# Kernel optimization log

Measured on AMD Instinct MI355X. Metric: run time of the kernel, lower is better.

## Reference

```python
import jax, jax.numpy as jnp
import numpy as np

H, W = 200, 200           # BEV spatial shape (single level)
NBQ, NH, NL, NP = 2, 8, 1, 4
D = 256
HD = D // NH


def setup_inputs() -> dict:
    key = jax.random.key(0)
    ks = jax.random.split(key, 12)
    bs, nq = 1, H * W
    query = jax.random.normal(ks[0], (bs, nq, D), jnp.float32)
    value = jax.random.normal(ks[1], (bs, NBQ * nq, D), jnp.float32)
    reference_points = jax.random.uniform(ks[2], (bs, nq, NL, 2), dtype=jnp.float32)
    spatial_shapes = jnp.array([[H, W]], dtype=jnp.int32)
    sc = 1.0 / np.sqrt(D)
    W_v = jax.random.normal(ks[3], (D, D), jnp.float32) * sc
    b_v = jax.random.normal(ks[4], (D,), jnp.float32) * 0.01
    W_so = jax.random.normal(ks[5], (2 * D, NBQ * NH * NL * NP * 2), jnp.float32) * 0.02
    b_so = jax.random.normal(ks[6], (NBQ * NH * NL * NP * 2,), jnp.float32) * 0.5
    W_aw = jax.random.normal(ks[7], (2 * D, NBQ * NH * NL * NP), jnp.float32) * 0.02
    b_aw = jax.random.normal(ks[8], (NBQ * NH * NL * NP,), jnp.float32) * 0.01
    W_o = jax.random.normal(ks[9], (D, D), jnp.float32) * sc
    b_o = jax.random.normal(ks[10], (D,), jnp.float32) * 0.01
    return {"query": query, "value": value, "reference_points": reference_points,
            "spatial_shapes": spatial_shapes,
            "W_v": W_v, "b_v": b_v, "W_so": W_so, "b_so": b_so,
            "W_aw": W_aw, "b_aw": b_aw, "W_o": W_o, "b_o": b_o}


def _ms_deform_attn(value, locs, attn):
    # value: (B, K, NH, HD); locs: (B, nq, NH, NL, NP, 2) in [0,1]; attn: (B, nq, NH, NL, NP)
    B, K, h, d = value.shape
    nq = locs.shape[1]
    out = jnp.zeros((B, nq, h, d), value.dtype)
    start = 0
    for l, (Hl, Wl) in enumerate([(H, W)]):
        v = value[:, start:start + Hl * Wl].transpose(0, 2, 1, 3).reshape(B * h, Hl * Wl, d)
        start += Hl * Wl
        g = locs[:, :, :, l]                      # (B, nq, h, NP, 2)
        # grid_sample(align_corners=False, padding='zeros') pixel coords
        x = g[..., 0] * Wl - 0.5
        y = g[..., 1] * Hl - 0.5
        x0 = jnp.floor(x); y0 = jnp.floor(y)
        lx = x - x0; ly = y - y0
        x0 = x0.astype(jnp.int32); y0 = y0.astype(jnp.int32)
        acc = jnp.zeros((B * h, nq * NP, d), value.dtype)
        for dy, wy in ((0, 1.0 - ly), (1, ly)):
            for dx, wx in ((0, 1.0 - lx), (1, lx)):
                xi = x0 + dx; yi = y0 + dy
                valid = ((xi >= 0) & (xi < Wl) & (yi >= 0) & (yi < Hl)).astype(value.dtype)
                idx = jnp.clip(yi, 0, Hl - 1) * Wl + jnp.clip(xi, 0, Wl - 1)  # (B,nq,h,NP)
                idxf = idx.transpose(0, 2, 1, 3).reshape(B * h, nq * NP)
                samp = jnp.take_along_axis(v, idxf[:, :, None], axis=1)       # (B*h, nq*NP, d)
                wgt = (wx * wy * valid).transpose(0, 2, 1, 3).reshape(B * h, nq * NP, 1)
                acc = acc + samp * wgt
        acc = acc.reshape(B, h, nq, NP, d)
        out = out + jnp.einsum('bhqpd,bqhp->bqhd', acc, attn[:, :, :, l])
    return out.reshape(B, nq, h * d)


def reference(query, value, reference_points, spatial_shapes,
              W_v, b_v, W_so, b_so, W_aw, b_aw, W_o, b_o):
    bs, nq, _ = query.shape
    identity = query
    val4 = value.reshape(bs, NBQ, nq, D)
    # query enhanced with most recent bev-queue features
    qe = jnp.concatenate([val4[:, 0], query], axis=-1)           # (bs, nq, 2D)
    vproj = (value @ W_v + b_v).reshape(bs * NBQ, nq, NH, HD)
    off = (qe @ W_so + b_so).reshape(bs, nq, NH, NBQ, NL, NP, 2)
    aw = (qe @ W_aw + b_aw).reshape(bs, nq, NH, NBQ, NL * NP)
    aw = jax.nn.softmax(aw, axis=-1).reshape(bs, nq, NH, NBQ, NL, NP)
    aw = aw.transpose(0, 3, 1, 2, 4, 5).reshape(bs * NBQ, nq, NH, NL, NP)
    # offset normalizer: [W, H] per level
    norm = jnp.stack([spatial_shapes[:, 1], spatial_shapes[:, 0]], -1).astype(query.dtype)  # (NL,2)
    locs = (reference_points[:, :, None, None, :, None, :]
            + off / norm[None, None, None, None, :, None, :])     # (bs,nq,NH,NBQ,NL,NP,2)
    locs = locs.transpose(0, 3, 1, 2, 4, 5, 6).reshape(bs * NBQ, nq, NH, NL, NP, 2)
    out = _ms_deform_attn(vproj, locs, aw)                        # (bs*NBQ, nq, D)
    out = out.reshape(bs, NBQ, nq, D).mean(axis=1)
    return out @ W_o + b_o + identity
```

## Files before the change

kernel.cpp:

```cpp
#include <hip/hip_runtime.h>
#include <math.h>

#define HW_   40000
#define NQ_   40000
#define IMGW  200
#define IMGH  200

typedef __bf16 bf16;
typedef __attribute__((ext_vector_type(4))) __bf16 bf16x4;
typedef __attribute__((ext_vector_type(8))) __bf16 bf16x8;
typedef __attribute__((ext_vector_type(4))) float f32x4;

__device__ __forceinline__ void gload_lds16(const void* g, void* l) {
  __builtin_amdgcn_global_load_lds(
      (const __attribute__((address_space(1))) void*)g,
      (__attribute__((address_space(3))) void*)l, 16, 0, 0);
}

__global__ __launch_bounds__(256) void prep_kernel(
    const float* __restrict__ value, const float* __restrict__ query,
    const float* __restrict__ Wv, const float* __restrict__ Wso,
    const float* __restrict__ Waw, const float* __restrict__ Wo,
    bf16* __restrict__ vbf, bf16* __restrict__ qbf,
    bf16* __restrict__ BtV, bf16* __restrict__ BtOA, bf16* __restrict__ BtO)
{
  const int b = blockIdx.x;
  if (b < 15000) {
    const float* src = (b < 10000) ? value : query;
    bf16* dst        = (b < 10000) ? vbf : qbf;
    int i = (b < 10000 ? b : b - 10000) * 256 + threadIdx.x;
    const float4 a = ((const float4*)src)[2 * i];
    const float4 c = ((const float4*)src)[2 * i + 1];
    bf16x8 o = {(bf16)a.x, (bf16)a.y, (bf16)a.z, (bf16)a.w,
                (bf16)c.x, (bf16)c.y, (bf16)c.z, (bf16)c.w};
    *(bf16x8*)&dst[(size_t)i * 8] = o;
    return;
  }
  int idx = (b - 15000) * 256 + threadIdx.x;
  if (idx < 65536) {
    int k = idx >> 8, n = idx & 255;
    BtV[(size_t)n * 256 + k] = (bf16)Wv[idx];
  } else if (idx < 131072) {
    int j = idx - 65536;
    int k = j >> 7, n = j & 127;
    BtOA[(size_t)n * 512 + k] = (bf16)Wso[j];
  } else if (idx < 163840) {
    int j = idx - 131072;
    int k = j >> 6, n = j & 63;
    BtOA[(size_t)(128 + n) * 512 + k] = (bf16)Waw[j];
  } else if (idx < 229376) {
    int j = idx - 163840;
    int k = j >> 8, n = j & 255;
    BtO[(size_t)n * 256 + k] = (bf16)Wo[j];
  }
}

template<int KT, int MODE, int BN>
__global__ __launch_bounds__(256) void mfma_gemm_kernel(
    const bf16* __restrict__ A0, const bf16* __restrict__ A1,
    const bf16* __restrict__ Bt,
    const float* __restrict__ bias0, const float* __restrict__ bias1,
    const float* __restrict__ resid,
    void* __restrict__ outp, void* __restrict__ outp2, int M)
{
  constexpr int NT16 = BN / 32;
  constexpr int BCH  = BN / 64;
  __shared__ bf16 As[2][128 * 32];
  __shared__ bf16 Bs[2][BN * 32];
  const int t    = threadIdx.x;
  const int m0   = blockIdx.x * 128;
  const int w    = t >> 6;
  const int lane = t & 63;
  const int quad = lane >> 4;
  const int l16  = lane & 15;
  const int wm   = (w & 1) * 64;
  const int wn   = (w >> 1) * (BN / 2);

  f32x4 acc[4][NT16] = {};

  int gmA[2];
#pragma unroll
  for (int i = 0; i < 2; ++i) {
    int gm = m0 + ((i * 256 + t) >> 2);
    gmA[i] = (gm >= M) ? (M - 1) : gm;
  }

  auto issue = [&](int it) {
    const int kt  = it * 32;
    const int buf = it & 1;
    const bf16* Ap;
    int col;
    if (KT == 512) { Ap = (kt < 256) ? A0 : A1; col = kt & 255; }
    else           { Ap = A0; col = kt; }
#pragma unroll
    for (int i = 0; i < 2; ++i) {
      int c = i * 256 + t;
      gload_lds16(&Ap[(size_t)gmA[i] * 256 + col + (c & 3) * 8], &As[buf][c * 8]);
    }
#pragma unroll
    for (int i = 0; i < BCH; ++i) {
      int c = i * 256 + t;
      gload_lds16(&Bt[(size_t)(c >> 2) * KT + kt + (c & 3) * 8], &Bs[buf][c * 8]);
    }
  };

  constexpr int NIT = KT / 32;
  issue(0);
#pragma unroll
  for (int it = 0; it < NIT; ++it) {
    __syncthreads();
    if (it + 1 < NIT) issue(it + 1);
    const bf16* as = As[it & 1];
    const bf16* bs = Bs[it & 1];
    bf16x8 af[4], bfr[NT16];
#pragma unroll
    for (int x = 0; x < 4; ++x)
      af[x] = *(const bf16x8*)&as[(wm + x * 16 + l16) * 32 + quad * 8];
#pragma unroll
    for (int x = 0; x < NT16; ++x)
      bfr[x] = *(const bf16x8*)&bs[(wn + x * 16 + l16) * 32 + quad * 8];
#pragma unroll
    for (int mt = 0; mt < 4; ++mt)
#pragma unroll
      for (int nt = 0; nt < NT16; ++nt)
        acc[mt][nt] = __builtin_amdgcn_mfma_f32_16x16x32_bf16(
            af[mt], bfr[nt], acc[mt][nt], 0, 0, 0);
  }

#pragma unroll
  for (int mt = 0; mt < 4; ++mt) {
#pragma unroll
    for (int r = 0; r < 4; ++r) {
      const int gm = m0 + wm + mt * 16 + quad * 4 + r;
      if (gm >= M) continue;
#pragma unroll
      for (int nt = 0; nt < NT16; ++nt) {
        const int gn = wn + nt * 16 + l16;
        float v = acc[mt][nt][r];
        if (MODE == 0) {
          int nbq = (gm >= HW_) ? 1 : 0;
          int pix = gm - nbq * HW_;
          int h = gn >> 5, hd = gn & 31;
          ((bf16*)outp)[(((size_t)(nbq * 8 + h) * HW_ + pix) << 5) + hd] =
              (bf16)(v + bias0[gn]);
        } else if (MODE == 1) {
          if (gn < 128)
            ((bf16*)outp)[(size_t)gm * 128 + gn] = (bf16)(v + bias0[gn]);
          else
            ((bf16*)outp2)[(size_t)gm * 64 + (gn - 128)] =
                (bf16)(v + bias1[gn - 128]);
        } else {
          ((float*)outp)[(size_t)gm * 256 + gn] =
              v + bias0[gn] + resid[(size_t)gm * 256 + gn];
        }
      }
    }
  }
}

__global__ __launch_bounds__(256) void deform_attn_kernel(
    const bf16* __restrict__ vws,
    const bf16* __restrict__ off_bf,
    const bf16* __restrict__ aw_bf,
    const float* __restrict__ ref,
    bf16* __restrict__ ms)
{
  const int t    = threadIdx.x;
  const int w    = t >> 6;
  const int lane = t & 63;
  const int h    = blockIdx.x & 7;
  const int qb   = blockIdx.x >> 3;
  const int qi   = lane >> 3;
  const int q    = qb * 32 + w * 8 + qi;
  const int nbq  = (lane >> 2) & 1;
  const int sub  = lane & 3;
  const int g    = h * 2 + nbq;

  const float rx = ref[2 * q + 0] * (float)IMGW - 0.5f;
  const float ry = ref[2 * q + 1] * (float)IMGH - 0.5f;

  bf16x4 a4 = *(const bf16x4*)&aw_bf[(size_t)q * 64 + g * 4];
  float aa0 = (float)a4[0], aa1 = (float)a4[1], aa2 = (float)a4[2], aa3 = (float)a4[3];
  float mx = fmaxf(fmaxf(aa0, aa1), fmaxf(aa2, aa3));
  float e0 = __expf(aa0 - mx), e1 = __expf(aa1 - mx);
  float e2 = __expf(aa2 - mx), e3 = __expf(aa3 - mx);
  float inv = 1.0f / (e0 + e1 + e2 + e3);
  float w4[4] = {e0 * inv, e1 * inv, e2 * inv, e3 * inv};

  bf16x8 o8 = *(const bf16x8*)&off_bf[(size_t)q * 128 + g * 8];
  float ox[4] = {(float)o8[0], (float)o8[2], (float)o8[4], (float)o8[6]};
  float oy[4] = {(float)o8[1], (float)o8[3], (float)o8[5], (float)o8[7]};

  const bf16* vbase = vws + (((size_t)(nbq * 8 + h) * HW_) << 5) + sub * 8;

  float acc[8] = {};
#pragma unroll
  for (int p = 0; p < 4; ++p) {
    float x = rx + ox[p];
    float y = ry + oy[p];
    float xf = floorf(x), yf = floorf(y);
    int   x0 = (int)xf,   y0 = (int)yf;
    float lx = x - xf,    ly = y - yf;
    int   x1 = x0 + 1,    y1 = y0 + 1;
    float w00 = (1.0f - lx) * (1.0f - ly);
    float w01 = lx * (1.0f - ly);
    float w10 = (1.0f - lx) * ly;
    float w11 = lx * ly;
    if (x0 < 0 || x0 >= IMGW) { w00 = 0.0f; w10 = 0.0f; }
    if (x1 < 0 || x1 >= IMGW) { w01 = 0.0f; w11 = 0.0f; }
    if (y0 < 0 || y0 >= IMGH) { w00 = 0.0f; w01 = 0.0f; }
    if (y1 < 0 || y1 >= IMGH) { w10 = 0.0f; w11 = 0.0f; }
    int xc0 = min(max(x0, 0), IMGW - 1), xc1 = min(max(x1, 0), IMGW - 1);
    int yc0 = min(max(y0, 0), IMGH - 1), yc1 = min(max(y1, 0), IMGH - 1);
    bf16x8 v00 = *(const bf16x8*)&vbase[(size_t)(yc0 * IMGW + xc0) << 5];
    bf16x8 v01 = *(const bf16x8*)&vbase[(size_t)(yc0 * IMGW + xc1) << 5];
    bf16x8 v10 = *(const bf16x8*)&vbase[(size_t)(yc1 * IMGW + xc0) << 5];
    bf16x8 v11 = *(const bf16x8*)&vbase[(size_t)(yc1 * IMGW + xc1) << 5];
    float wp = w4[p];
#pragma unroll
    for (int j = 0; j < 8; ++j) {
      float s = w00 * (float)v00[j] + w01 * (float)v01[j] +
                w10 * (float)v10[j] + w11 * (float)v11[j];
      acc[j] = fmaf(wp, s, acc[j]);
    }
  }

#pragma unroll
  for (int j = 0; j < 8; ++j) acc[j] += __shfl_xor(acc[j], 4);

  if (nbq == 0) {
    bf16x8 o;
#pragma unroll
    for (int j = 0; j < 8; ++j) o[j] = (bf16)(0.5f * acc[j]);
    *(bf16x8*)&ms[(size_t)q * 256 + h * 32 + sub * 8] = o;
  }
}

extern "C" void kernel_launch(void* const* d_in, const int* in_sizes, int n_in,
                              void* d_out, int out_size, void* d_ws, size_t ws_size,
                              hipStream_t stream) {
  const float* query = (const float*)d_in[0];
  const float* value = (const float*)d_in[1];
  const float* ref   = (const float*)d_in[2];
  const float* Wv  = (const float*)d_in[4];
  const float* bv  = (const float*)d_in[5];
  const float* Wso = (const float*)d_in[6];
  const float* bso = (const float*)d_in[7];
  const float* Waw = (const float*)d_in[8];
  const float* baw = (const float*)d_in[9];
  const float* Wo  = (const float*)d_in[10];
  const float* bo  = (const float*)d_in[11];
  float* out = (float*)d_out;

  char* p = (char*)d_ws;
  bf16* vws    = (bf16*)p; p += (size_t)2 * 8 * HW_ * 32 * 2;
  bf16* off_bf = (bf16*)p; p += (size_t)NQ_ * 128 * 2;
  bf16* aw_bf  = (bf16*)p; p += (size_t)NQ_ * 64 * 2;
  bf16* ms     = (bf16*)p; p += (size_t)NQ_ * 256 * 2;
  bf16* vbf    = (bf16*)p; p += (size_t)2 * HW_ * 256 * 2;
  bf16* qbf    = (bf16*)p; p += (size_t)NQ_ * 256 * 2;
  bf16* BtV    = (bf16*)p; p += (size_t)256 * 256 * 2;
  bf16* BtOA   = (bf16*)p; p += (size_t)192 * 512 * 2;
  bf16* BtO    = (bf16*)p; p += (size_t)256 * 256 * 2;

  prep_kernel<<<15896, 256, 0, stream>>>(value, query, Wv, Wso, Waw, Wo,
                                         vbf, qbf, BtV, BtOA, BtO);

  mfma_gemm_kernel<256, 0, 256><<<625, 256, 0, stream>>>(
      vbf, nullptr, BtV, bv, nullptr, nullptr, vws, nullptr, 2 * HW_);
  mfma_gemm_kernel<512, 1, 192><<<313, 256, 0, stream>>>(
      vbf, qbf, BtOA, bso, baw, nullptr, off_bf, aw_bf, NQ_);
  deform_attn_kernel<<<10000, 256, 0, stream>>>(vws, off_bf, aw_bf, ref, ms);
  mfma_gemm_kernel<256, 2, 256><<<313, 256, 0, stream>>>(
      ms, nullptr, BtO, bo, nullptr, query, out, nullptr, NQ_);
}
```

Before: 312.6 us.

## Fuse fp32-to-bf16 activation conversion into GEMM A-tile loads

Removes the separate pass that converted value and query to bf16 buffers in prep_kernel. The first two GEMMs now read fp32 activations straight into registers, convert them, and write bf16 into LDS, with the next tile's loads prefetched while the current MFMAs run. This drops one full read and write of the activations and their workspace buffers. In exchange, the GEMMs read twice as many A bytes and lose the asynchronous global-to-LDS load path for A, which adds register pressure and VALU conversion work.

```diff
diff --git a/kernel.cpp b/kernel.cpp
--- a/kernel.cpp
+++ b/kernel.cpp
@@ -18,25 +18,11 @@
 }
 
 __global__ __launch_bounds__(256) void prep_kernel(
-    const float* __restrict__ value, const float* __restrict__ query,
     const float* __restrict__ Wv, const float* __restrict__ Wso,
     const float* __restrict__ Waw, const float* __restrict__ Wo,
-    bf16* __restrict__ vbf, bf16* __restrict__ qbf,
     bf16* __restrict__ BtV, bf16* __restrict__ BtOA, bf16* __restrict__ BtO)
 {
-  const int b = blockIdx.x;
-  if (b < 15000) {
-    const float* src = (b < 10000) ? value : query;
-    bf16* dst        = (b < 10000) ? vbf : qbf;
-    int i = (b < 10000 ? b : b - 10000) * 256 + threadIdx.x;
-    const float4 a = ((const float4*)src)[2 * i];
-    const float4 c = ((const float4*)src)[2 * i + 1];
-    bf16x8 o = {(bf16)a.x, (bf16)a.y, (bf16)a.z, (bf16)a.w,
-                (bf16)c.x, (bf16)c.y, (bf16)c.z, (bf16)c.w};
-    *(bf16x8*)&dst[(size_t)i * 8] = o;
-    return;
-  }
-  int idx = (b - 15000) * 256 + threadIdx.x;
+  int idx = blockIdx.x * 256 + threadIdx.x;
   if (idx < 65536) {
     int k = idx >> 8, n = idx & 255;
     BtV[(size_t)n * 256 + k] = (bf16)Wv[idx];
@@ -55,9 +41,9 @@
   }
 }
 
-template<int KT, int MODE, int BN>
+template<int KT, int MODE, int BN, int AF32>
 __global__ __launch_bounds__(256) void mfma_gemm_kernel(
-    const bf16* __restrict__ A0, const bf16* __restrict__ A1,
+    const void* __restrict__ A0, const void* __restrict__ A1,
     const bf16* __restrict__ Bt,
     const float* __restrict__ bias0, const float* __restrict__ bias1,
     const float* __restrict__ resid,
@@ -85,31 +71,71 @@
     gmA[i] = (gm >= M) ? (M - 1) : gm;
   }
 
-  auto issue = [&](int it) {
+  float4 apf[2][2];
+
+  auto issueB = [&](int it) {
+    const int kt  = it * 32;
+    const int buf = it & 1;
+#pragma unroll
+    for (int i = 0; i < BCH; ++i) {
+      int c = i * 256 + t;
+      gload_lds16(&Bt[(size_t)(c >> 2) * KT + kt + (c & 3) * 8], &Bs[buf][c * 8]);
+    }
+  };
+
+  auto issueA_lds = [&](int it) {
     const int kt  = it * 32;
     const int buf = it & 1;
     const bf16* Ap;
     int col;
-    if (KT == 512) { Ap = (kt < 256) ? A0 : A1; col = kt & 255; }
-    else           { Ap = A0; col = kt; }
+    if (KT == 512) { Ap = (kt < 256) ? (const bf16*)A0 : (const bf16*)A1; col = kt & 255; }
+    else           { Ap = (const bf16*)A0; col = kt; }
 #pragma unroll
     for (int i = 0; i < 2; ++i) {
       int c = i * 256 + t;
       gload_lds16(&Ap[(size_t)gmA[i] * 256 + col + (c & 3) * 8], &As[buf][c * 8]);
     }
-#pragma unroll
-    for (int i = 0; i < BCH; ++i) {
+  };
+
+  auto loadA_f32 = [&](int it) {
+    const int kt = it * 32;
+    const float* Ap;
+    int col;
+    if (KT == 512) { Ap = (kt < 256) ? (const float*)A0 : (const float*)A1; col = kt & 255; }
+    else           { Ap = (const float*)A0; col = kt; }
+#pragma unroll
+    for (int i = 0; i < 2; ++i) {
       int c = i * 256 + t;
-      gload_lds16(&Bt[(size_t)(c >> 2) * KT + kt + (c & 3) * 8], &Bs[buf][c * 8]);
+      const float4* s = (const float4*)&Ap[(size_t)gmA[i] * 256 + col + (c & 3) * 8];
+      apf[i][0] = s[0];
+      apf[i][1] = s[1];
     }
   };
 
+  auto writeA = [&](int it) {
+    const int buf = it & 1;
+#pragma unroll
+    for (int i = 0; i < 2; ++i) {
+      int c = i * 256 + t;
+      bf16x8 o = {(bf16)apf[i][0].x, (bf16)apf[i][0].y,
+                  (bf16)apf[i][0].z, (bf16)apf[i][0].w,
+                  (bf16)apf[i][1].x, (bf16)apf[i][1].y,
+                  (bf16)apf[i][1].z, (bf16)apf[i][1].w};
+      *(bf16x8*)&As[buf][c * 8] = o;
+    }
+  };
+
   constexpr int NIT = KT / 32;
-  issue(0);
+  if (AF32) { loadA_f32(0); issueB(0); writeA(0); }
+  else      { issueA_lds(0); issueB(0); }
+
 #pragma unroll
   for (int it = 0; it < NIT; ++it) {
     __syncthreads();
-    if (it + 1 < NIT) issue(it + 1);
+    if (it + 1 < NIT) {
+      issueB(it + 1);
+      if (AF32) loadA_f32(it + 1); else issueA_lds(it + 1);
+    }
     const bf16* as = As[it & 1];
     const bf16* bs = Bs[it & 1];
     bf16x8 af[4], bfr[NT16];
@@ -125,6 +151,7 @@
       for (int nt = 0; nt < NT16; ++nt)
         acc[mt][nt] = __builtin_amdgcn_mfma_f32_16x16x32_bf16(
             af[mt], bfr[nt], acc[mt][nt], 0, 0, 0);
+    if (AF32 && it + 1 < NIT) writeA(it + 1);
   }
 
 #pragma unroll
@@ -257,20 +284,17 @@
   bf16* off_bf = (bf16*)p; p += (size_t)NQ_ * 128 * 2;
   bf16* aw_bf  = (bf16*)p; p += (size_t)NQ_ * 64 * 2;
   bf16* ms     = (bf16*)p; p += (size_t)NQ_ * 256 * 2;
-  bf16* vbf    = (bf16*)p; p += (size_t)2 * HW_ * 256 * 2;
-  bf16* qbf    = (bf16*)p; p += (size_t)NQ_ * 256 * 2;
   bf16* BtV    = (bf16*)p; p += (size_t)256 * 256 * 2;
   bf16* BtOA   = (bf16*)p; p += (size_t)192 * 512 * 2;
   bf16* BtO    = (bf16*)p; p += (size_t)256 * 256 * 2;
 
-  prep_kernel<<<15896, 256, 0, stream>>>(value, query, Wv, Wso, Waw, Wo,
-                                         vbf, qbf, BtV, BtOA, BtO);
-
-  mfma_gemm_kernel<256, 0, 256><<<625, 256, 0, stream>>>(
-      vbf, nullptr, BtV, bv, nullptr, nullptr, vws, nullptr, 2 * HW_);
-  mfma_gemm_kernel<512, 1, 192><<<313, 256, 0, stream>>>(
-      vbf, qbf, BtOA, bso, baw, nullptr, off_bf, aw_bf, NQ_);
+  prep_kernel<<<896, 256, 0, stream>>>(Wv, Wso, Waw, Wo, BtV, BtOA, BtO);
+
+  mfma_gemm_kernel<256, 0, 256, 1><<<625, 256, 0, stream>>>(
+      value, nullptr, BtV, bv, nullptr, nullptr, vws, nullptr, 2 * HW_);
+  mfma_gemm_kernel<512, 1, 192, 1><<<313, 256, 0, stream>>>(
+      value, query, BtOA, bso, baw, nullptr, off_bf, aw_bf, NQ_);
   deform_attn_kernel<<<10000, 256, 0, stream>>>(vws, off_bf, aw_bf, ref, ms);
-  mfma_gemm_kernel<256, 2, 256><<<313, 256, 0, stream>>>(
+  mfma_gemm_kernel<256, 2, 256, 0><<<313, 256, 0, stream>>>(
       ms, nullptr, BtO, bo, nullptr, query, out, nullptr, NQ_);
 }
```

Measured after the change: 305.6 us. 1.02x faster.
